# Kernel optimization log

Measured on AMD Instinct MI355X. Metric: run time of the kernel, lower is better.

## Reference

```python
import jax, jax.numpy as jnp
import numpy as np
import math

N, D, F = 8192, 512, 2048
M, K = 4096, 128  # masked cells, masked genes per cell
EPS = 1e-5


def setup_inputs() -> dict:
    key = jax.random.key(0)
    ks = jax.random.split(key, 16)
    s = 0.02
    x = jax.random.normal(ks[0], (N, D), jnp.float32)
    # distinct masked cell indices (torch.randperm semantics)
    mask_nodes = jax.random.permutation(ks[1], N)[:M].astype(jnp.int64)
    # per-row distinct gene indices (torch.randperm per row)
    gene_idx = jnp.argsort(jax.random.uniform(ks[2], (M, D)), axis=1)[:, :K].astype(jnp.int64)
    return {
        'x': x, 'mask_nodes': mask_nodes, 'gene_idx': gene_idx,
        'Wq_e': s * jax.random.normal(ks[3], (D, D), jnp.float32),
        'Wk_e': s * jax.random.normal(ks[4], (D, D), jnp.float32),
        'Wv_e': s * jax.random.normal(ks[5], (D, D), jnp.float32),
        'ln1_g': jnp.ones((D,), jnp.float32), 'ln1_b': jnp.zeros((D,), jnp.float32),
        'ff_W1': s * jax.random.normal(ks[6], (D, F), jnp.float32),
        'ff_b1': jnp.zeros((F,), jnp.float32),
        'ff_W2': s * jax.random.normal(ks[7], (F, D), jnp.float32),
        'ff_b2': jnp.zeros((D,), jnp.float32),
        'ln2_g': jnp.ones((D,), jnp.float32), 'ln2_b': jnp.zeros((D,), jnp.float32),
        'Wq_d': s * jax.random.normal(ks[8], (D, D), jnp.float32),
        'Wk_d': s * jax.random.normal(ks[9], (D, D), jnp.float32),
        'Wv_d': s * jax.random.normal(ks[10], (D, D), jnp.float32),
        'ln3_g': jnp.ones((D,), jnp.float32), 'ln3_b': jnp.zeros((D,), jnp.float32),
        'ln4_g': jnp.ones((D,), jnp.float32), 'ln4_b': jnp.zeros((D,), jnp.float32),
        'head_W': s * jax.random.normal(ks[11], (D, D), jnp.float32),
        'head_b': jnp.zeros((D,), jnp.float32),
    }


def _ln(h, g, b):
    mu = jnp.mean(h, axis=-1, keepdims=True)
    var = jnp.mean(jnp.square(h - mu), axis=-1, keepdims=True)
    return (h - mu) * jax.lax.rsqrt(var + EPS) * g + b


def _attn(h, Wq, Wk, Wv):
    Q = h @ Wq
    Kt = h @ Wk
    V = h @ Wv
    scores = (Q @ Kt.T) / math.sqrt(D)  # [N, N]
    attn = jax.nn.softmax(scores, axis=-1)
    return attn @ V, attn


def _ff(h, W1, b1, W2, b2):
    return jax.nn.gelu(h @ W1 + b1, approximate=False) @ W2 + b2


def reference(x, mask_nodes, gene_idx,
              Wq_e, Wk_e, Wv_e, ln1_g, ln1_b,
              ff_W1, ff_b1, ff_W2, ff_b2, ln2_g, ln2_b,
              Wq_d, Wk_d, Wv_d, ln3_g, ln3_b, ln4_g, ln4_b,
              head_W, head_b):
    # mask selected genes of selected cells to 0 (encoding_mask_nodes)
    rows = mask_nodes[:, None]
    use_x = x.at[rows, gene_idx].set(0.0)

    hidden, encode_weights = _attn(use_x, Wq_e, Wk_e, Wv_e)
    hidden = _ln(hidden + use_x, ln1_g, ln1_b)
    hidden = _ln(hidden + _ff(hidden, ff_W1, ff_b1, ff_W2, ff_b2), ln2_g, ln2_b)
    # NOTE: `hidden[mask_nodes][gene_mask] = 0` in the original torch code
    # writes into a copy produced by advanced indexing -> it is a no-op.

    recon, _ = _attn(hidden, Wq_d, Wk_d, Wv_d)
    recon = _ln(recon + hidden, ln3_g, ln3_b)
    # original reuses self.ff (not self.ff1) in the decoder block
    recon = _ln(recon + _ff(recon, ff_W1, ff_b1, ff_W2, ff_b2), ln4_g, ln4_b)
    h = recon @ head_W + head_b

    x_init = x[rows, gene_idx]      # [M, K]
    x_recon = h[rows, gene_idx]     # [M, K]
    return (x_init, x_recon, encode_weights, recon)
```

## Files before the change

### kernel.cpp

```cpp
#include <hip/hip_runtime.h>
#include <hip/hip_bf16.h>
#include <stdint.h>
#include <math.h>

typedef __bf16 bf16_t;
typedef __bf16 bf16x8 __attribute__((ext_vector_type(8)));
typedef __bf16 bf16x4 __attribute__((ext_vector_type(4)));
typedef float floatx4 __attribute__((ext_vector_type(4)));

#define NN 8192
#define DD 512
#define FF 2048
#define MM 4096
#define KK 128

__device__ __forceinline__ void async_copy16(const void* g, void* l) {
    __builtin_amdgcn_global_load_lds(
        (const __attribute__((address_space(1))) void*)(uintptr_t)g,
        (__attribute__((address_space(3))) void*)(uint32_t)(uintptr_t)l,
        16, 0, 0);
}

template<int EPI, typename OT>
__global__ __launch_bounds__(256)
void gemm_nt(const bf16_t* __restrict__ A, const bf16_t* __restrict__ B,
             OT* __restrict__ C, OT* __restrict__ C2,
             int M, int Nc, int Kd, int ldA, int ldB, int ldC,
             float scale, const float* __restrict__ bias,
             float* __restrict__ denom)
{
    __shared__ bf16_t As[128 * 32];
    __shared__ bf16_t Bs[128 * 32];

    const int tid  = threadIdx.x;
    const int lane = tid & 63;
    const int wave = tid >> 6;
    const int wm   = (wave >> 1) << 6;
    const int wn   = (wave & 1) << 6;
    const int quad = lane >> 4;
    const int l16  = lane & 15;

    const int gx   = gridDim.x;
    const int nwg  = gx * gridDim.y;
    const int orig = blockIdx.y * gx + blockIdx.x;
    const int swz  = (orig & 7) * (nwg >> 3) + (orig >> 3);
    const long bm  = (long)(swz % gx) * 128;
    const long bn  = (long)(swz / gx) * 128;

    const int  kchunk = Kd / gridDim.z;
    const long kBeg   = (long)blockIdx.z * kchunk;
    OT* __restrict__ Co = blockIdx.z ? C2 : C;

    const int t0 = tid, t1 = tid + 256;
    const bf16_t* pA0 = A + (bm + (t0 >> 2)) * (long)ldA + (t0 & 3) * 8 + kBeg;
    const bf16_t* pA1 = A + (bm + (t1 >> 2)) * (long)ldA + (t1 & 3) * 8 + kBeg;
    const bf16_t* pB0 = B + (bn + (t0 >> 2)) * (long)ldB + (t0 & 3) * 8 + kBeg;
    const bf16_t* pB1 = B + (bn + (t1 >> 2)) * (long)ldB + (t1 & 3) * 8 + kBeg;
    bf16_t* lA0 = &As[t0 * 8];
    bf16_t* lA1 = &As[t1 * 8];
    bf16_t* lB0 = &Bs[t0 * 8];
    bf16_t* lB1 = &Bs[t1 * 8];

    floatx4 acc[4][4] = {};

    for (long k0 = 0; k0 < kchunk; k0 += 32) {
        async_copy16(pA0 + k0, lA0);
        async_copy16(pA1 + k0, lA1);
        async_copy16(pB0 + k0, lB0);
        async_copy16(pB1 + k0, lB1);
        __syncthreads();

        bf16x8 af[4], bfr[4];
#pragma unroll
        for (int i = 0; i < 4; i++) {
            af[i]  = *(const bf16x8*)&As[(wm + i * 16 + l16) * 32 + quad * 8];
            bfr[i] = *(const bf16x8*)&Bs[(wn + i * 16 + l16) * 32 + quad * 8];
        }
#pragma unroll
        for (int mi = 0; mi < 4; mi++)
#pragma unroll
            for (int ni = 0; ni < 4; ni++)
                acc[mi][ni] = __builtin_amdgcn_mfma_f32_16x16x32_bf16(
                    af[mi], bfr[ni], acc[mi][ni], 0, 0, 0);
        __syncthreads();
    }

#pragma unroll
    for (int mi = 0; mi < 4; mi++) {
        const long rbase = bm + wm + mi * 16 + quad * 4;
        if (EPI == 4) {
#pragma unroll
            for (int r = 0; r < 4; r++) {
                float rsum = 0.0f;
#pragma unroll
                for (int ni = 0; ni < 4; ni++) {
                    const long col = bn + wn + ni * 16 + l16;
                    float v = __expf(acc[mi][ni][r] * scale);
                    rsum += v;
                    Co[(rbase + r) * (long)ldC + col] = (OT)v;
                }
                rsum += __shfl_xor(rsum, 1);
                rsum += __shfl_xor(rsum, 2);
                rsum += __shfl_xor(rsum, 4);
                rsum += __shfl_xor(rsum, 8);
                if (l16 == 0) atomicAdd(denom + rbase + r, rsum);
            }
        } else {
#pragma unroll
            for (int ni = 0; ni < 4; ni++) {
                const long col = bn + wn + ni * 16 + l16;
                float bv = (EPI >= 2) ? bias[col] : 0.0f;
#pragma unroll
                for (int r = 0; r < 4; r++) {
                    float v = acc[mi][ni][r];
                    if (EPI == 1) v *= scale;
                    if (EPI >= 2) v += bv;
                    if (EPI == 3) v = 0.5f * v * (1.0f + erff(v * 0.70710678118f));
                    Co[(rbase + r) * (long)ldC + col] = (OT)v;
                }
            }
        }
    }
}

template<int EPI, typename OT>
static void launch_gemm(const bf16_t* A, const bf16_t* B, OT* C, OT* C2,
                        int M, int Nc, int Kd, int lda, int ldb, int ldc,
                        int splitk, float scale, const float* bias,
                        float* denom, hipStream_t s)
{
    dim3 g(M / 128, Nc / 128, splitk);
    gemm_nt<EPI, OT><<<g, 256, 0, s>>>(A, B, C, C2, M, Nc, Kd, lda, ldb, ldc,
                                       scale, bias, denom);
}

__global__ __launch_bounds__(256)
void transpose_f2b(const float* __restrict__ in, bf16_t* __restrict__ out,
                   int R, int C)
{
    __shared__ float tile[32][33];
    const int bx = blockIdx.x * 32;
    const int by = blockIdx.y * 32;
    const int tx = threadIdx.x, ty = threadIdx.y;
#pragma unroll
    for (int i = 0; i < 32; i += 8)
        tile[ty + i][tx] = in[(long)(by + ty + i) * C + bx + tx];
    __syncthreads();
#pragma unroll
    for (int i = 0; i < 32; i += 8)
        out[(long)(bx + ty + i) * R + by + tx] = (bf16_t)tile[tx][ty + i];
}

__global__ __launch_bounds__(256)
void transpose_b2b(const bf16_t* __restrict__ in, bf16_t* __restrict__ out,
                   int R, int C, int ldin)
{
    __shared__ bf16_t tile[32][34];
    const int bx = blockIdx.x * 32;
    const int by = blockIdx.y * 32;
    const int tx = threadIdx.x, ty = threadIdx.y;
#pragma unroll
    for (int i = 0; i < 32; i += 8)
        tile[ty + i][tx] = in[(long)(by + ty + i) * ldin + bx + tx];
    __syncthreads();
#pragma unroll
    for (int i = 0; i < 32; i += 8)
        out[(long)(bx + ty + i) * R + by + tx] = tile[tx][ty + i];
}

__global__ __launch_bounds__(256)
void encw_norm(const bf16_t* __restrict__ P, const float* __restrict__ denom,
               float* __restrict__ out)
{
    const long row = blockIdx.x;
    const float inv = 1.0f / denom[row];
    const bf16_t* p = P + row * (long)NN;
    float* q = out + row * (long)NN;
    const int tid = threadIdx.x;
#pragma unroll
    for (int i = 0; i < 4; i++) {
        const int o = (tid + i * 256) * 8;
        bf16x8 v = *(const bf16x8*)(p + o);
        float4 lo, hi;
        lo.x = (float)v[0] * inv; lo.y = (float)v[1] * inv;
        lo.z = (float)v[2] * inv; lo.w = (float)v[3] * inv;
        hi.x = (float)v[4] * inv; hi.y = (float)v[5] * inv;
        hi.z = (float)v[6] * inv; hi.w = (float)v[7] * inv;
        *(float4*)(q + o)     = lo;
        *(float4*)(q + o + 4) = hi;
    }
}

__global__ __launch_bounds__(256)
void zero_f32(float* __restrict__ p)
{
    p[blockIdx.x * 256 + threadIdx.x] = 0.0f;
}

template<bool RS, bool CB>
__global__ __launch_bounds__(64)
void add_ln_gen(const float* __restrict__ a, const float* __restrict__ a2,
                const float* __restrict__ rs, const float* __restrict__ cb,
                const float* __restrict__ b,
                const float* __restrict__ g, const float* __restrict__ be,
                bf16_t* __restrict__ ob, float* __restrict__ of)
{
    const long row = blockIdx.x;
    const int lane = threadIdx.x;
    const long base = row * DD + lane * 8;
    const float irs = RS ? (1.0f / rs[row]) : 1.0f;
    float v[8], s = 0.0f, s2 = 0.0f;
#pragma unroll
    for (int j = 0; j < 8; j++) {
        float t = (a[base + j] + a2[base + j]) * irs;
        if (CB) t += cb[lane * 8 + j];
        t += b[base + j];
        v[j] = t;
        s += t; s2 += t * t;
    }
#pragma unroll
    for (int off = 32; off > 0; off >>= 1) {
        s  += __shfl_xor(s,  off);
        s2 += __shfl_xor(s2, off);
    }
    const float mu  = s * (1.0f / DD);
    const float var = s2 * (1.0f / DD) - mu * mu;
    const float inv = rsqrtf(var + 1e-5f);
    bf16x8 o;
#pragma unroll
    for (int j = 0; j < 8; j++) {
        float r = (v[j] - mu) * inv * g[lane * 8 + j] + be[lane * 8 + j];
        o[j] = (bf16_t)r;
        of[base + j] = r;
    }
    *(bf16x8*)(ob + base) = o;
}

__global__ __launch_bounds__(256)
void build_usex(const float* __restrict__ x, bf16_t* __restrict__ ub,
                float* __restrict__ uf)
{
    const long i = ((long)blockIdx.x * 256 + threadIdx.x) * 4;
    const float4 v = *(const float4*)(x + i);
    *(float4*)(uf + i) = v;
    bf16x4 o = { (bf16_t)v.x, (bf16_t)v.y, (bf16_t)v.z, (bf16_t)v.w };
    *(bf16x4*)(ub + i) = o;
}

__global__ __launch_bounds__(256)
void scatter_zero(bf16_t* __restrict__ ub, float* __restrict__ uf,
                  const int* __restrict__ mn, const int* __restrict__ gi)
{
    const int i = blockIdx.x * 256 + threadIdx.x;
    const long idx = (long)mn[i >> 7] * DD + gi[i];
    ub[idx] = (bf16_t)0.0f;
    uf[idx] = 0.0f;
}

__global__ __launch_bounds__(256)
void gather_mk(const float* __restrict__ src, const int* __restrict__ mn,
               const int* __restrict__ gi, float* __restrict__ dst)
{
    const int i = blockIdx.x * 256 + threadIdx.x;
    dst[i] = src[(long)mn[i >> 7] * DD + gi[i]];
}

__global__ __launch_bounds__(256)
void gather_head(const float* __restrict__ p1, const float* __restrict__ p2,
                 const float* __restrict__ hb, const int* __restrict__ mn,
                 const int* __restrict__ gi, float* __restrict__ dst)
{
    const int i = blockIdx.x * 256 + threadIdx.x;
    const int col = gi[i];
    const long idx = (long)mn[i >> 7] * DD + col;
    dst[i] = p1[idx] + p2[idx] + hb[col];
}

extern "C" void kernel_launch(void* const* d_in, const int* in_sizes, int n_in,
                              void* d_out, int out_size, void* d_ws, size_t ws_size,
                              hipStream_t stream)
{
    const float* x      = (const float*)d_in[0];
    const int*   mn     = (const int*)d_in[1];
    const int*   gi     = (const int*)d_in[2];
    const float* Wq_e   = (const float*)d_in[3];
    const float* Wk_e   = (const float*)d_in[4];
    const float* Wv_e   = (const float*)d_in[5];
    const float* ln1_g  = (const float*)d_in[6];
    const float* ln1_b  = (const float*)d_in[7];
    const float* ff_W1  = (const float*)d_in[8];
    const float* ff_b1  = (const float*)d_in[9];
    const float* ff_W2  = (const float*)d_in[10];
    const float* ff_b2  = (const float*)d_in[11];
    const float* ln2_g  = (const float*)d_in[12];
    const float* ln2_b  = (const float*)d_in[13];
    const float* Wq_d   = (const float*)d_in[14];
    const float* Wk_d   = (const float*)d_in[15];
    const float* Wv_d   = (const float*)d_in[16];
    const float* ln3_g  = (const float*)d_in[17];
    const float* ln3_b  = (const float*)d_in[18];
    const float* ln4_g  = (const float*)d_in[19];
    const float* ln4_b  = (const float*)d_in[20];
    const float* head_W = (const float*)d_in[21];
    const float* head_b = (const float*)d_in[22];

    float* outf     = (float*)d_out;
    float* o_xinit  = outf;
    float* o_xrecon = outf + (size_t)MM * KK;
    float* o_encw   = outf + (size_t)2 * MM * KK;
    float* o_recon  = o_encw + (size_t)NN * NN;

    char* ws = (char*)d_ws;
    size_t off = 0;
    auto alloc = [&](size_t bytes) -> void* {
        void* p = ws + off;
        off += (bytes + 255) & ~(size_t)255;
        return p;
    };
    const size_t NDb = (size_t)NN * DD * sizeof(bf16_t);
    const size_t NDf = (size_t)NN * DD * sizeof(float);

    bf16_t* usex_b = (bf16_t*)alloc(NDb);
    bf16_t* qkv_b  = (bf16_t*)alloc((size_t)NN * 3 * DD * 2);
    bf16_t* vt_b   = (bf16_t*)alloc(NDb);
    bf16_t* hid_b  = (bf16_t*)alloc(NDb);
    float*  usex_f = (float*)alloc(NDf);
    float*  resA_f = (float*)alloc(NDf);
    float*  gout_f = (float*)alloc(NDf);
    bf16_t* wt_qe  = (bf16_t*)alloc((size_t)DD * DD * 2);
    bf16_t* wt_ke  = (bf16_t*)alloc((size_t)DD * DD * 2);
    bf16_t* wt_ve  = (bf16_t*)alloc((size_t)DD * DD * 2);
    bf16_t* wt_qd  = (bf16_t*)alloc((size_t)DD * DD * 2);
    bf16_t* wt_kd  = (bf16_t*)alloc((size_t)DD * DD * 2);
    bf16_t* wt_vd  = (bf16_t*)alloc((size_t)DD * DD * 2);
    bf16_t* wt_h   = (bf16_t*)alloc((size_t)DD * DD * 2);
    bf16_t* w1t    = (bf16_t*)alloc((size_t)DD * FF * 2);
    bf16_t* w2t    = (bf16_t*)alloc((size_t)FF * DD * 2);
    float*  denom  = (float*)alloc((size_t)NN * sizeof(float));
    bf16_t* scores = (bf16_t*)alloc((size_t)NN * NN * 2);
    bf16_t* t1_b   = scores;
    float*  resB_f = usex_f;
    float*  pv2_f  = (float*)qkv_b;
    (void)ws_size; (void)in_sizes; (void)n_in; (void)out_size;
    (void)wt_ke; (void)wt_ve; (void)wt_kd; (void)wt_vd;

    auto tr = [&](const float* in, bf16_t* o, int R, int C) {
        transpose_f2b<<<dim3(C / 32, R / 32), dim3(32, 8), 0, stream>>>(in, o, R, C);
    };
    const float SC = 0.04419417382f;

    tr(Wq_e, wt_qe, DD, DD);  tr(Wk_e, wt_ke, DD, DD);  tr(Wv_e, wt_ve, DD, DD);
    tr(Wq_d, wt_qd, DD, DD);  tr(Wk_d, wt_kd, DD, DD);  tr(Wv_d, wt_vd, DD, DD);
    tr(head_W, wt_h, DD, DD); tr(ff_W1, w1t, DD, FF);   tr(ff_W2, w2t, FF, DD);

    build_usex<<<NN * DD / 1024, 256, 0, stream>>>(x, usex_b, usex_f);
    scatter_zero<<<MM * KK / 256, 256, 0, stream>>>(usex_b, usex_f, mn, gi);
    gather_mk<<<MM * KK / 256, 256, 0, stream>>>(x, mn, gi, o_xinit);

    launch_gemm<0, bf16_t>(usex_b, wt_qe, qkv_b, nullptr,
                           NN, 3 * DD, DD, DD, DD, 3 * DD, 1, 0.f, nullptr,
                           nullptr, stream);
    transpose_b2b<<<dim3(DD / 32, NN / 32), dim3(32, 8), 0, stream>>>(
        qkv_b + 2 * DD, vt_b, NN, DD, 3 * DD);
    zero_f32<<<NN / 256, 256, 0, stream>>>(denom);
    launch_gemm<4, bf16_t>(qkv_b, qkv_b + DD, scores, nullptr,
                           NN, NN, DD, 3 * DD, 3 * DD, NN, 1, SC, nullptr,
                           denom, stream);
    encw_norm<<<NN, 256, 0, stream>>>(scores, denom, o_encw);
    launch_gemm<0, float>(scores, vt_b, gout_f, pv2_f,
                          NN, DD, NN, NN, NN, DD, 2, 0.f, nullptr,
                          nullptr, stream);
    add_ln_gen<true, false><<<NN, 64, 0, stream>>>(
        gout_f, pv2_f, denom, nullptr, usex_f, ln1_g, ln1_b, hid_b, resA_f);

    launch_gemm<3, bf16_t>(hid_b, w1t, t1_b, nullptr,
                           NN, FF, DD, DD, DD, FF, 1, 0.f, ff_b1,
                           nullptr, stream);
    launch_gemm<0, float>(t1_b, w2t, gout_f, pv2_f,
                          NN, DD, FF, FF, FF, DD, 2, 0.f, nullptr,
                          nullptr, stream);
    add_ln_gen<false, true><<<NN, 64, 0, stream>>>(
        gout_f, pv2_f, nullptr, ff_b2, resA_f, ln2_g, ln2_b, hid_b, resB_f);

    launch_gemm<0, bf16_t>(hid_b, wt_qd, qkv_b, nullptr,
                           NN, 3 * DD, DD, DD, DD, 3 * DD, 1, 0.f, nullptr,
                           nullptr, stream);
    transpose_b2b<<<dim3(DD / 32, NN / 32), dim3(32, 8), 0, stream>>>(
        qkv_b + 2 * DD, vt_b, NN, DD, 3 * DD);
    zero_f32<<<NN / 256, 256, 0, stream>>>(denom);
    launch_gemm<4, bf16_t>(qkv_b, qkv_b + DD, scores, nullptr,
                           NN, NN, DD, 3 * DD, 3 * DD, NN, 1, SC, nullptr,
                           denom, stream);
    launch_gemm<0, float>(scores, vt_b, gout_f, pv2_f,
                          NN, DD, NN, NN, NN, DD, 2, 0.f, nullptr,
                          nullptr, stream);
    add_ln_gen<true, false><<<NN, 64, 0, stream>>>(
        gout_f, pv2_f, denom, nullptr, resB_f, ln3_g, ln3_b, hid_b, resA_f);

    launch_gemm<3, bf16_t>(hid_b, w1t, t1_b, nullptr,
                           NN, FF, DD, DD, DD, FF, 1, 0.f, ff_b1,
                           nullptr, stream);
    launch_gemm<0, float>(t1_b, w2t, gout_f, pv2_f,
                          NN, DD, FF, FF, FF, DD, 2, 0.f, nullptr,
                          nullptr, stream);
    add_ln_gen<false, true><<<NN, 64, 0, stream>>>(
        gout_f, pv2_f, nullptr, ff_b2, resA_f, ln4_g, ln4_b, hid_b, o_recon);

    launch_gemm<0, float>(hid_b, wt_h, gout_f, pv2_f,
                          NN, DD, DD, DD, DD, DD, 2, 0.f, nullptr,
                          nullptr, stream);
    gather_head<<<MM * KK / 256, 256, 0, stream>>>(gout_f, pv2_f, head_b,
                                                   mn, gi, o_xrecon);
}
```

Baseline: 1.209 ms.

## Stage GEMM epilogue through LDS for coalesced stores; raise split-K to four

The GEMM epilogue now writes each 32x128 slab of results into shared memory first, then stores it to global memory as 16-byte vector rows, replacing scattered per-element stores. Split-K partial outputs now go to a strided buffer instead of two fixed pointers. This lets the PV and FF2 GEMMs (N=512) use four K-splits to fill more CUs, and the LayerNorm kernel sums all the partials. The cost is extra barriers in the epilogue and more partial-sum traffic, including a new 4x NxD float buffer.

Result: slower. 1.266 ms (+4.7%).

```diff
diff --git a/kernel.cpp b/kernel.cpp
--- a/kernel.cpp
+++ b/kernel.cpp
@@ -14,6 +14,10 @@
 #define MM 4096
 #define KK 128
 
+template<typename T> struct V16;
+template<> struct V16<bf16_t> { using t = bf16x8;  static const int sh = 3; };
+template<> struct V16<float>  { using t = floatx4; static const int sh = 2; };
+
 __device__ __forceinline__ void async_copy16(const void* g, void* l) {
     __builtin_amdgcn_global_load_lds(
         (const __attribute__((address_space(1))) void*)(uintptr_t)g,
@@ -24,13 +28,14 @@
 template<int EPI, typename OT>
 __global__ __launch_bounds__(256)
 void gemm_nt(const bf16_t* __restrict__ A, const bf16_t* __restrict__ B,
-             OT* __restrict__ C, OT* __restrict__ C2,
+             OT* __restrict__ C,
              int M, int Nc, int Kd, int ldA, int ldB, int ldC,
-             float scale, const float* __restrict__ bias,
+             long partStride, float scale, const float* __restrict__ bias,
              float* __restrict__ denom)
 {
-    __shared__ bf16_t As[128 * 32];
-    __shared__ bf16_t Bs[128 * 32];
+    __shared__ char smem[16384];
+    bf16_t* As = (bf16_t*)smem;
+    bf16_t* Bs = (bf16_t*)(smem + 8192);
 
     const int tid  = threadIdx.x;
     const int lane = tid & 63;
@@ -49,7 +54,7 @@
 
     const int  kchunk = Kd / gridDim.z;
     const long kBeg   = (long)blockIdx.z * kchunk;
-    OT* __restrict__ Co = blockIdx.z ? C2 : C;
+    OT* __restrict__ Co = C + (long)blockIdx.z * partStride;
 
     const int t0 = tid, t1 = tid + 256;
     const bf16_t* pA0 = A + (bm + (t0 >> 2)) * (long)ldA + (t0 & 3) * 8 + kBeg;
@@ -85,8 +90,11 @@
         __syncthreads();
     }
 
+    OT* sm = (OT*)smem;
+    const int g = wm >> 6;
 #pragma unroll
     for (int mi = 0; mi < 4; mi++) {
+        if (mi) __syncthreads();
         const long rbase = bm + wm + mi * 16 + quad * 4;
         if (EPI == 4) {
 #pragma unroll
@@ -94,10 +102,9 @@
                 float rsum = 0.0f;
 #pragma unroll
                 for (int ni = 0; ni < 4; ni++) {
-                    const long col = bn + wn + ni * 16 + l16;
                     float v = __expf(acc[mi][ni][r] * scale);
                     rsum += v;
-                    Co[(rbase + r) * (long)ldC + col] = (OT)v;
+                    sm[(g * 16 + quad * 4 + r) * 128 + wn + ni * 16 + l16] = (OT)v;
                 }
                 rsum += __shfl_xor(rsum, 1);
                 rsum += __shfl_xor(rsum, 2);
@@ -108,30 +115,43 @@
         } else {
 #pragma unroll
             for (int ni = 0; ni < 4; ni++) {
-                const long col = bn + wn + ni * 16 + l16;
-                float bv = (EPI >= 2) ? bias[col] : 0.0f;
+                float bv = (EPI >= 2) ? bias[bn + wn + ni * 16 + l16] : 0.0f;
 #pragma unroll
                 for (int r = 0; r < 4; r++) {
                     float v = acc[mi][ni][r];
                     if (EPI == 1) v *= scale;
                     if (EPI >= 2) v += bv;
                     if (EPI == 3) v = 0.5f * v * (1.0f + erff(v * 0.70710678118f));
-                    Co[(rbase + r) * (long)ldC + col] = (OT)v;
+                    sm[(g * 16 + quad * 4 + r) * 128 + wn + ni * 16 + l16] = (OT)v;
                 }
             }
         }
+        __syncthreads();
+        typedef typename V16<OT>::t VT;
+        const int VSH = V16<OT>::sh;
+        const int VEC = 1 << VSH;
+        const int NP  = (32 * 128) / (256 * VEC);
+#pragma unroll
+        for (int p = 0; p < NP; p++) {
+            const int vid  = p * 256 + tid;
+            const int lrow = vid >> (7 - VSH);
+            const int vcol = vid & ((128 >> VSH) - 1);
+            const long grow = bm + (lrow >> 4) * 64 + mi * 16 + (lrow & 15);
+            *(VT*)&Co[grow * (long)ldC + bn + vcol * VEC] =
+                *(const VT*)&sm[lrow * 128 + vcol * VEC];
+        }
     }
 }
 
 template<int EPI, typename OT>
-static void launch_gemm(const bf16_t* A, const bf16_t* B, OT* C, OT* C2,
+static void launch_gemm(const bf16_t* A, const bf16_t* B, OT* C,
                         int M, int Nc, int Kd, int lda, int ldb, int ldc,
-                        int splitk, float scale, const float* bias,
-                        float* denom, hipStream_t s)
+                        int splitk, long partStride, float scale,
+                        const float* bias, float* denom, hipStream_t s)
 {
     dim3 g(M / 128, Nc / 128, splitk);
-    gemm_nt<EPI, OT><<<g, 256, 0, s>>>(A, B, C, C2, M, Nc, Kd, lda, ldb, ldc,
-                                       scale, bias, denom);
+    gemm_nt<EPI, OT><<<g, 256, 0, s>>>(A, B, C, M, Nc, Kd, lda, ldb, ldc,
+                                       partStride, scale, bias, denom);
 }
 
 __global__ __launch_bounds__(256)
@@ -197,9 +217,9 @@
     p[blockIdx.x * 256 + threadIdx.x] = 0.0f;
 }
 
-template<bool RS, bool CB>
+template<int NP, bool RS, bool CB>
 __global__ __launch_bounds__(64)
-void add_ln_gen(const float* __restrict__ a, const float* __restrict__ a2,
+void add_ln_gen(const float* __restrict__ a, long pstride,
                 const float* __restrict__ rs, const float* __restrict__ cb,
                 const float* __restrict__ b,
                 const float* __restrict__ g, const float* __restrict__ be,
@@ -212,7 +232,10 @@
     float v[8], s = 0.0f, s2 = 0.0f;
 #pragma unroll
     for (int j = 0; j < 8; j++) {
-        float t = (a[base + j] + a2[base + j]) * irs;
+        float t = 0.0f;
+#pragma unroll
+        for (int p = 0; p < NP; p++) t += a[base + j + p * pstride];
+        t *= irs;
         if (CB) t += cb[lane * 8 + j];
         t += b[base + j];
         v[j] = t;
@@ -266,14 +289,14 @@
 }
 
 __global__ __launch_bounds__(256)
-void gather_head(const float* __restrict__ p1, const float* __restrict__ p2,
+void gather_head(const float* __restrict__ p1, long pstride,
                  const float* __restrict__ hb, const int* __restrict__ mn,
                  const int* __restrict__ gi, float* __restrict__ dst)
 {
     const int i = blockIdx.x * 256 + threadIdx.x;
     const int col = gi[i];
     const long idx = (long)mn[i >> 7] * DD + col;
-    dst[i] = p1[idx] + p2[idx] + hb[col];
+    dst[i] = p1[idx] + p1[idx + pstride] + hb[col];
 }
 
 extern "C" void kernel_launch(void* const* d_in, const int* in_sizes, int n_in,
@@ -319,6 +342,7 @@
     };
     const size_t NDb = (size_t)NN * DD * sizeof(bf16_t);
     const size_t NDf = (size_t)NN * DD * sizeof(float);
+    const long   NDe = (long)NN * DD;
 
     bf16_t* usex_b = (bf16_t*)alloc(NDb);
     bf16_t* qkv_b  = (bf16_t*)alloc((size_t)NN * 3 * DD * 2);
@@ -326,7 +350,7 @@
     bf16_t* hid_b  = (bf16_t*)alloc(NDb);
     float*  usex_f = (float*)alloc(NDf);
     float*  resA_f = (float*)alloc(NDf);
-    float*  gout_f = (float*)alloc(NDf);
+    float*  part_f = (float*)alloc(4 * NDf);
     bf16_t* wt_qe  = (bf16_t*)alloc((size_t)DD * DD * 2);
     bf16_t* wt_ke  = (bf16_t*)alloc((size_t)DD * DD * 2);
     bf16_t* wt_ve  = (bf16_t*)alloc((size_t)DD * DD * 2);
@@ -340,7 +364,6 @@
     bf16_t* scores = (bf16_t*)alloc((size_t)NN * NN * 2);
     bf16_t* t1_b   = scores;
     float*  resB_f = usex_f;
-    float*  pv2_f  = (float*)qkv_b;
     (void)ws_size; (void)in_sizes; (void)n_in; (void)out_size;
     (void)wt_ke; (void)wt_ve; (void)wt_kd; (void)wt_vd;
 
@@ -357,58 +380,58 @@
     scatter_zero<<<MM * KK / 256, 256, 0, stream>>>(usex_b, usex_f, mn, gi);
     gather_mk<<<MM * KK / 256, 256, 0, stream>>>(x, mn, gi, o_xinit);
 
-    launch_gemm<0, bf16_t>(usex_b, wt_qe, qkv_b, nullptr,
-                           NN, 3 * DD, DD, DD, DD, 3 * DD, 1, 0.f, nullptr,
+    launch_gemm<0, bf16_t>(usex_b, wt_qe, qkv_b,
+                           NN, 3 * DD, DD, DD, DD, 3 * DD, 1, 0, 0.f, nullptr,
                            nullptr, stream);
     transpose_b2b<<<dim3(DD / 32, NN / 32), dim3(32, 8), 0, stream>>>(
         qkv_b + 2 * DD, vt_b, NN, DD, 3 * DD);
     zero_f32<<<NN / 256, 256, 0, stream>>>(denom);
-    launch_gemm<4, bf16_t>(qkv_b, qkv_b + DD, scores, nullptr,
-                           NN, NN, DD, 3 * DD, 3 * DD, NN, 1, SC, nullptr,
+    launch_gemm<4, bf16_t>(qkv_b, qkv_b + DD, scores,
+                           NN, NN, DD, 3 * DD, 3 * DD, NN, 1, 0, SC, nullptr,
                            denom, stream);
     encw_norm<<<NN, 256, 0, stream>>>(scores, denom, o_encw);
-    launch_gemm<0, float>(scores, vt_b, gout_f, pv2_f,
-                          NN, DD, NN, NN, NN, DD, 2, 0.f, nullptr,
+    launch_gemm<0, float>(scores, vt_b, part_f,
+                          NN, DD, NN, NN, NN, DD, 4, NDe, 0.f, nullptr,
                           nullptr, stream);
-    add_ln_gen<true, false><<<NN, 64, 0, stream>>>(
-        gout_f, pv2_f, denom, nullptr, usex_f, ln1_g, ln1_b, hid_b, resA_f);
-
-    launch_gemm<3, bf16_t>(hid_b, w1t, t1_b, nullptr,
-                           NN, FF, DD, DD, DD, FF, 1, 0.f, ff_b1,
+    add_ln_gen<4, true, false><<<NN, 64, 0, stream>>>(
+        part_f, NDe, denom, nullptr, usex_f, ln1_g, ln1_b, hid_b, resA_f);
+
+    launch_gemm<3, bf16_t>(hid_b, w1t, t1_b,
+                           NN, FF, DD, DD, DD, FF, 1, 0, 0.f, ff_b1,
                            nullptr, stream);
-    launch_gemm<0, float>(t1_b, w2t, gout_f, pv2_f,
-                          NN, DD, FF, FF, FF, DD, 2, 0.f, nullptr,
+    launch_gemm<0, float>(t1_b, w2t, part_f,
+                          NN, DD, FF, FF, FF, DD, 4, NDe, 0.f, nullptr,
                           nullptr, stream);
-    add_ln_gen<false, true><<<NN, 64, 0, stream>>>(
-        gout_f, pv2_f, nullptr, ff_b2, resA_f, ln2_g, ln2_b, hid_b, resB_f);
-
-    launch_gemm<0, bf16_t>(hid_b, wt_qd, qkv_b, nullptr,
-                           NN, 3 * DD, DD, DD, DD, 3 * DD, 1, 0.f, nullptr,
+    add_ln_gen<4, false, true><<<NN, 64, 0, stream>>>(
+        part_f, NDe, nullptr, ff_b2, resA_f, ln2_g, ln2_b, hid_b, resB_f);
+
+    launch_gemm<0, bf16_t>(hid_b, wt_qd, qkv_b,
+                           NN, 3 * DD, DD, DD, DD, 3 * DD, 1, 0, 0.f, nullptr,
                            nullptr, stream);
     transpose_b2b<<<dim3(DD / 32, NN / 32), dim3(32, 8), 0, stream>>>(
         qkv_b + 2 * DD, vt_b, NN, DD, 3 * DD);
     zero_f32<<<NN / 256, 256, 0, stream>>>(denom);
-    launch_gemm<4, bf16_t>(qkv_b, qkv_b + DD, scores, nullptr,
-                           NN, NN, DD, 3 * DD, 3 * DD, NN, 1, SC, nullptr,
+    launch_gemm<4, bf16_t>(qkv_b, qkv_b + DD, scores,
+                           NN, NN, DD, 3 * DD, 3 * DD, NN, 1, 0, SC, nullptr,
                            denom, stream);
-    launch_gemm<0, float>(scores, vt_b, gout_f, pv2_f,
-                          NN, DD, NN, NN, NN, DD, 2, 0.f, nullptr,
+    launch_gemm<0, float>(scores, vt_b, part_f,
+                          NN, DD, NN, NN, NN, DD, 4, NDe, 0.f, nullptr,
                           nullptr, stream);
-    add_ln_gen<true, false><<<NN, 64, 0, stream>>>(
-        gout_f, pv2_f, denom, nullptr, resB_f, ln3_g, ln3_b, hid_b, resA_f);
-
-    launch_gemm<3, bf16_t>(hid_b, w1t, t1_b, nullptr,
-                           NN, FF, DD, DD, DD, FF, 1, 0.f, ff_b1,
+    add_ln_gen<4, true, false><<<NN, 64, 0, stream>>>(
+        part_f, NDe, denom, nullptr, resB_f, ln3_g, ln3_b, hid_b, resA_f);
+
+    launch_gemm<3, bf16_t>(hid_b, w1t, t1_b,
+                           NN, FF, DD, DD, DD, FF, 1, 0, 0.f, ff_b1,
                            nullptr, stream);
-    launch_gemm<0, float>(t1_b, w2t, gout_f, pv2_f,
-                          NN, DD, FF, FF, FF, DD, 2, 0.f, nullptr,
+    launch_gemm<0, float>(t1_b, w2t, part_f,
+                          NN, DD, FF, FF, FF, DD, 4, NDe, 0.f, nullptr,
                           nullptr, stream);
-    add_ln_gen<false, true><<<NN, 64, 0, stream>>>(
-        gout_f, pv2_f, nullptr, ff_b2, resA_f, ln4_g, ln4_b, hid_b, o_recon);
-
-    launch_gemm<0, float>(hid_b, wt_h, gout_f, pv2_f,
-                          NN, DD, DD, DD, DD, DD, 2, 0.f, nullptr,
+    add_ln_gen<4, false, true><<<NN, 64, 0, stream>>>(
+        part_f, NDe, nullptr, ff_b2, resA_f, ln4_g, ln4_b, hid_b, o_recon);
+
+    launch_gemm<0, float>(hid_b, wt_h, part_f,
+                          NN, DD, DD, DD, DD, DD, 2, NDe, 0.f, nullptr,
                           nullptr, stream);
-    gather_head<<<MM * KK / 256, 256, 0, stream>>>(gout_f, pv2_f, head_b,
+    gather_head<<<MM * KK / 256, 256, 0, stream>>>(part_f, NDe, head_b,
                                                    mn, gi, o_xrecon);
 }
```
